# Kernel optimization log

Hardware: AMD Instinct MI355X
Metric: run time of the kernel (lower is better)

## Reference

```python
import jax, jax.numpy as jnp
import numpy as np

DIM_QK = 1024


def setup_inputs() -> dict:
    key = jax.random.key(0)
    ks = jax.random.split(key, 5)
    B, S, D = 4, 2048, 1024
    return {
        "x": jax.random.normal(ks[0], (B, S, D), dtype=jnp.float32),
        "Wq": jax.random.normal(ks[1], (DIM_QK, D), dtype=jnp.float32) * (D ** -0.5),
        "Wk": jax.random.normal(ks[2], (DIM_QK, D), dtype=jnp.float32) * (D ** -0.5),
        "Wv": jax.random.normal(ks[3], (D, D), dtype=jnp.float32) * (D ** -0.5),
        "Wo": jax.random.normal(ks[4], (D, D), dtype=jnp.float32) * (D ** -0.5),
    }


def reference(x, Wq, Wk, Wv, Wo):
    # torch Linear: y = x @ W.T (no bias)
    q = jnp.einsum('bsd,kd->bsk', x, Wq)
    k = jnp.einsum('bsd,kd->bsk', x, Wk)
    v = jnp.einsum('bsd,vd->bsv', x, Wv)
    scale = (DIM_QK // 2) ** (-0.5)
    dist = jnp.einsum('bqk,btk->bqt', q, k) * scale  # [B,S,S]
    weight = jax.lax.stop_gradient(dist)             # pre-softmax scores (detached)
    attn = jax.nn.softmax(dist, axis=-1)
    ctx = jnp.einsum('bqt,btv->bqv', attn, v)
    out = jnp.einsum('bqv,ev->bqe', ctx, Wo)
    return (out, weight)
```

## Files before the change

kernel.cpp:

```cpp
#include <hip/hip_runtime.h>
#include <stdint.h>

typedef __attribute__((ext_vector_type(8))) short bf16x8;
typedef __attribute__((ext_vector_type(4))) float f32x4;

__device__ __forceinline__ unsigned short f32_to_bf16(float f) {
  union { float f; unsigned int u; } v; v.f = f;
  unsigned int u = v.u;
  u += 0x7fffu + ((u >> 16) & 1u);
  return (unsigned short)(u >> 16);
}

__device__ __forceinline__ void gload_lds16(const unsigned short* g, unsigned short* lds_p) {
  __builtin_amdgcn_global_load_lds(
      (const __attribute__((address_space(1))) unsigned int*)g,
      (__attribute__((address_space(3))) unsigned int*)lds_p,
      16, 0, 0);
}

template<int MODE>
__global__ __launch_bounds__(256, 4)
void gemm_bt(const unsigned short* __restrict__ A,
             const unsigned short* __restrict__ Bm,
             void* __restrict__ Cv,
             int M, int N, int K, int lda, int ldb, int ldc,
             long sA_, long sB_, long sC_,
             float scale)
{
  __shared__ unsigned short sA[2 * 128 * 32];
  __shared__ unsigned short sB[2 * 128 * 32];

  const int bz = blockIdx.z;
  const unsigned short* Ab = A + (long)bz * sA_;
  const unsigned short* Bb = Bm + (long)bz * sB_;

  const int nx = gridDim.x;
  const int nwg = nx * gridDim.y;
  const int f = blockIdx.y * nx + blockIdx.x;
  const int cpx = nwg >> 3;
  const int sw = (f & 7) * cpx + (f >> 3);
  const int m0 = (sw % nx) * 128;
  const int n0 = (sw / nx) * 128;

  const int t = threadIdx.x;
  const int lane = t & 63;
  const int w = t >> 6;
  const int wr = (w >> 1) * 64;
  const int wc = (w & 1) * 64;
  const int lrow = lane & 15;
  const int q8s = ((lane >> 4) ^ ((lrow >> 1) & 3)) * 8;

  const int row0 = t >> 2;
  const int kc0 = ((t & 3) ^ ((t >> 3) & 3)) * 8;
  const unsigned short* Ap = Ab + (long)(m0 + row0) * lda + kc0;
  const unsigned short* Bp = Bb + (long)(n0 + row0) * ldb + kc0;
  const long a64 = (long)lda * 64;
  const long b64 = (long)ldb * 64;

  f32x4 acc[4][4];
#pragma unroll
  for (int i = 0; i < 4; ++i)
#pragma unroll
    for (int j = 0; j < 4; ++j)
      acc[i][j] = (f32x4){0.f, 0.f, 0.f, 0.f};

  for (int k0 = 0; k0 < K; k0 += 64) {
    __syncthreads();
#pragma unroll
    for (int s = 0; s < 2; ++s) {
      const int gk = k0 + s * 32;
      gload_lds16(Ap + gk,       &sA[s * 4096 + t * 8]);
      gload_lds16(Ap + a64 + gk, &sA[s * 4096 + t * 8 + 2048]);
      gload_lds16(Bp + gk,       &sB[s * 4096 + t * 8]);
      gload_lds16(Bp + b64 + gk, &sB[s * 4096 + t * 8 + 2048]);
    }
    __syncthreads();

#pragma unroll
    for (int s = 0; s < 2; ++s) {
      bf16x8 af[4], bf[4];
#pragma unroll
      for (int i = 0; i < 4; ++i) {
        af[i] = *(const bf16x8*)&sA[s * 4096 + (wr + i * 16 + lrow) * 32 + q8s];
        bf[i] = *(const bf16x8*)&sB[s * 4096 + (wc + i * 16 + lrow) * 32 + q8s];
      }
#pragma unroll
      for (int mi = 0; mi < 4; ++mi)
#pragma unroll
        for (int ni = 0; ni < 4; ++ni)
          acc[mi][ni] = __builtin_amdgcn_mfma_f32_16x16x32_bf16(af[mi], bf[ni], acc[mi][ni], 0, 0, 0);
    }
  }

  const int cl = lane & 15;
  const int rq = (lane >> 4) * 4;

  if (MODE == 2) {
    float* Cb = (float*)Cv + (long)bz * sC_;
#pragma unroll
    for (int mi = 0; mi < 4; ++mi) {
      const int rowb = m0 + wr + mi * 16 + rq;
#pragma unroll
      for (int ni = 0; ni < 4; ++ni) {
        const int col = n0 + wc + ni * 16 + cl;
#pragma unroll
        for (int r = 0; r < 4; ++r)
          Cb[(long)(rowb + r) * ldc + col] = acc[mi][ni][r] * scale;
      }
    }
  } else {
    unsigned short* Cb = (unsigned short*)Cv + (long)bz * sC_;
#pragma unroll
    for (int mi = 0; mi < 4; ++mi) {
      const int rowb = m0 + wr + mi * 16 + rq;
#pragma unroll
      for (int ni = 0; ni < 4; ++ni) {
        const int col = n0 + wc + ni * 16 + cl;
#pragma unroll
        for (int r = 0; r < 4; ++r)
          Cb[(long)(rowb + r) * ldc + col] = f32_to_bf16(acc[mi][ni][r]);
      }
    }
  }
}

__global__ __launch_bounds__(256)
void softmax_rows(const float* __restrict__ dist, unsigned short* __restrict__ attn) {
  const long row = blockIdx.x;
  const float4* in = (const float4*)(dist + row * 2048);
  const int t = threadIdx.x;
  float4 v0 = in[t];
  float4 v1 = in[t + 256];

  float m = fmaxf(fmaxf(fmaxf(v0.x, v0.y), fmaxf(v0.z, v0.w)),
                  fmaxf(fmaxf(v1.x, v1.y), fmaxf(v1.z, v1.w)));
#pragma unroll
  for (int off = 32; off > 0; off >>= 1)
    m = fmaxf(m, __shfl_xor(m, off, 64));

  __shared__ float redm[4];
  __shared__ float reds[4];
  if ((t & 63) == 0) redm[t >> 6] = m;
  __syncthreads();
  m = fmaxf(fmaxf(redm[0], redm[1]), fmaxf(redm[2], redm[3]));

  float e[8];
  e[0] = __expf(v0.x - m); e[1] = __expf(v0.y - m);
  e[2] = __expf(v0.z - m); e[3] = __expf(v0.w - m);
  e[4] = __expf(v1.x - m); e[5] = __expf(v1.y - m);
  e[6] = __expf(v1.z - m); e[7] = __expf(v1.w - m);

  float s = ((e[0] + e[1]) + (e[2] + e[3])) + ((e[4] + e[5]) + (e[6] + e[7]));
#pragma unroll
  for (int off = 32; off > 0; off >>= 1)
    s += __shfl_xor(s, off, 64);
  if ((t & 63) == 0) reds[t >> 6] = s;
  __syncthreads();
  s = (reds[0] + reds[1]) + (reds[2] + reds[3]);

  const float inv = 1.0f / s;
  ushort4 o0, o1;
  o0.x = f32_to_bf16(e[0] * inv); o0.y = f32_to_bf16(e[1] * inv);
  o0.z = f32_to_bf16(e[2] * inv); o0.w = f32_to_bf16(e[3] * inv);
  o1.x = f32_to_bf16(e[4] * inv); o1.y = f32_to_bf16(e[5] * inv);
  o1.z = f32_to_bf16(e[6] * inv); o1.w = f32_to_bf16(e[7] * inv);
  *(ushort4*)(attn + row * 2048 + t * 4) = o0;
  *(ushort4*)(attn + row * 2048 + 1024 + t * 4) = o1;
}

__global__ __launch_bounds__(256)
void cast_all(const float* __restrict__ Wq, const float* __restrict__ Wk,
              const float* __restrict__ Wv, const float* __restrict__ Wo,
              const float* __restrict__ x, unsigned short* __restrict__ dst) {
  const long i = ((long)blockIdx.x * 256 + threadIdx.x) * 4;
  const float* src;
  long off;
  if (i < 4194304) {
    const int which = (int)(i >> 20);
    src = (which == 0) ? Wq : (which == 1) ? Wk : (which == 2) ? Wv : Wo;
    off = i & 1048575;
  } else {
    src = x;
    off = i - 4194304;
  }
  float4 v = *(const float4*)(src + off);
  ushort4 o;
  o.x = f32_to_bf16(v.x); o.y = f32_to_bf16(v.y);
  o.z = f32_to_bf16(v.z); o.w = f32_to_bf16(v.w);
  *(ushort4*)(dst + i) = o;
}

extern "C" void kernel_launch(void* const* d_in, const int* in_sizes, int n_in,
                              void* d_out, int out_size, void* d_ws, size_t ws_size,
                              hipStream_t stream) {
  const float* x  = (const float*)d_in[0];
  const float* Wq = (const float*)d_in[1];
  const float* Wk = (const float*)d_in[2];
  const float* Wv = (const float*)d_in[3];
  const float* Wo = (const float*)d_in[4];

  const long Bn = 4, S = 2048, D = 1024;
  const long MS = Bn * S;

  float* out_p  = (float*)d_out;
  float* weight = out_p + MS * D;

  unsigned short* Wqb = (unsigned short*)d_ws;
  unsigned short* Wvb = Wqb + 2 * D * D;
  unsigned short* Wob = Wvb + D * D;
  unsigned short* xb  = Wob + D * D;
  unsigned short* qk  = xb + MS * D;
  unsigned short* vtb = qk + MS * 2048;
  unsigned short* attn = qk;
  unsigned short* ctx  = xb;

  cast_all<<<12288, 256, 0, stream>>>(Wq, Wk, Wv, Wo, x, Wqb);

  gemm_bt<0><<<dim3(64, 16, 1), 256, 0, stream>>>(xb, Wqb, qk, 8192, 2048, 1024,
                                                  1024, 1024, 2048, 0, 0, 0, 1.f);
  gemm_bt<0><<<dim3(8, 64, 1), 256, 0, stream>>>(Wvb, xb, vtb, 1024, 8192, 1024,
                                                 1024, 1024, 8192, 0, 0, 0, 1.f);
  gemm_bt<2><<<dim3(16, 16, 4), 256, 0, stream>>>(qk, qk + 1024, weight, 2048, 2048, 1024,
                                                  2048, 2048, 2048,
                                                  S * 2048, S * 2048, S * S,
                                                  0.04419417382415922f);
  softmax_rows<<<(int)(Bn * S), 256, 0, stream>>>(weight, attn);
  gemm_bt<0><<<dim3(16, 8, 4), 256, 0, stream>>>(attn, vtb, ctx, 2048, 1024, 2048,
                                                 2048, 8192, 1024,
                                                 S * S, 2048, S * D, 1.f);
  gemm_bt<2><<<dim3(64, 8, 1), 256, 0, stream>>>(ctx, Wob, out_p, 8192, 1024, 1024,
                                                 1024, 1024, 1024, 0, 0, 0, 1.f);
}
```

Baseline: 333.9 us.

## Stage GEMM epilogue through swizzled LDS for coalesced vector stores

The GEMM epilogue now swaps the MFMA operands so each lane holds four consecutive columns of one row. It stages the tile through a shared 32KB LDS buffer, with two passes for the fp32 mode, and then writes 16-byte coalesced vectors to global memory instead of scattered scalar stores. The XCD-aware block swizzle is removed and launch bounds drop from 4 to 2 waves per EU, presumably to fit the larger LDS footprint and extra registers. The price is extra barriers and LDS traffic in the epilogue, and possibly worse L2 locality across XCDs.

```diff
diff --git a/kernel.cpp b/kernel.cpp
--- a/kernel.cpp
+++ b/kernel.cpp
@@ -19,7 +19,7 @@
 }
 
 template<int MODE>
-__global__ __launch_bounds__(256, 4)
+__global__ __launch_bounds__(256, 2)
 void gemm_bt(const unsigned short* __restrict__ A,
              const unsigned short* __restrict__ Bm,
              void* __restrict__ Cv,
@@ -27,20 +27,16 @@
              long sA_, long sB_, long sC_,
              float scale)
 {
-  __shared__ unsigned short sA[2 * 128 * 32];
-  __shared__ unsigned short sB[2 * 128 * 32];
+  __shared__ unsigned short smem[16384];
+  unsigned short* sA = smem;
+  unsigned short* sB = smem + 8192;
 
   const int bz = blockIdx.z;
   const unsigned short* Ab = A + (long)bz * sA_;
   const unsigned short* Bb = Bm + (long)bz * sB_;
 
-  const int nx = gridDim.x;
-  const int nwg = nx * gridDim.y;
-  const int f = blockIdx.y * nx + blockIdx.x;
-  const int cpx = nwg >> 3;
-  const int sw = (f & 7) * cpx + (f >> 3);
-  const int m0 = (sw % nx) * 128;
-  const int n0 = (sw / nx) * 128;
+  const int m0 = blockIdx.x * 128;
+  const int n0 = blockIdx.y * 128;
 
   const int t = threadIdx.x;
   const int lane = t & 63;
@@ -88,38 +84,74 @@
       for (int mi = 0; mi < 4; ++mi)
 #pragma unroll
         for (int ni = 0; ni < 4; ++ni)
-          acc[mi][ni] = __builtin_amdgcn_mfma_f32_16x16x32_bf16(af[mi], bf[ni], acc[mi][ni], 0, 0, 0);
+          acc[mi][ni] = __builtin_amdgcn_mfma_f32_16x16x32_bf16(bf[ni], af[mi], acc[mi][ni], 0, 0, 0);
     }
   }
 
   const int cl = lane & 15;
   const int rq = (lane >> 4) * 4;
 
+  __syncthreads();
+
   if (MODE == 2) {
+    float* ef = (float*)smem;
     float* Cb = (float*)Cv + (long)bz * sC_;
 #pragma unroll
+    for (int pass = 0; pass < 2; ++pass) {
+      if ((w >> 1) == pass) {
+#pragma unroll
+        for (int mi = 0; mi < 4; ++mi) {
+          const int mr = mi * 16 + cl;
+#pragma unroll
+          for (int ni = 0; ni < 4; ++ni) {
+            const int n16 = (wc + ni * 16 + rq) >> 2;
+            const int ph = n16 ^ (mr & 15);
+            f32x4 v;
+            v[0] = acc[mi][ni][0] * scale; v[1] = acc[mi][ni][1] * scale;
+            v[2] = acc[mi][ni][2] * scale; v[3] = acc[mi][ni][3] * scale;
+            *(f32x4*)&ef[mr * 128 + ph * 4] = v;
+          }
+        }
+      }
+      __syncthreads();
+#pragma unroll
+      for (int i = 0; i < 8; ++i) {
+        const int c = t + i * 256;
+        const int m = c >> 5;
+        const int k16 = c & 31;
+        const int ph = k16 ^ (m & 15);
+        f32x4 v = *(const f32x4*)&ef[m * 128 + ph * 4];
+        *(f32x4*)&Cb[(long)(m0 + pass * 64 + m) * ldc + n0 + k16 * 4] = v;
+      }
+      __syncthreads();
+    }
+  } else {
+    unsigned short* eb = smem;
+    unsigned short* Cb = (unsigned short*)Cv + (long)bz * sC_;
+#pragma unroll
     for (int mi = 0; mi < 4; ++mi) {
-      const int rowb = m0 + wr + mi * 16 + rq;
+      const int mr = wr + mi * 16 + cl;
+      const int sw = (mr & 15) << 1;
 #pragma unroll
       for (int ni = 0; ni < 4; ++ni) {
-        const int col = n0 + wc + ni * 16 + cl;
-#pragma unroll
-        for (int r = 0; r < 4; ++r)
-          Cb[(long)(rowb + r) * ldc + col] = acc[mi][ni][r] * scale;
-      }
-    }
-  } else {
-    unsigned short* Cb = (unsigned short*)Cv + (long)bz * sC_;
-#pragma unroll
-    for (int mi = 0; mi < 4; ++mi) {
-      const int rowb = m0 + wr + mi * 16 + rq;
-#pragma unroll
-      for (int ni = 0; ni < 4; ++ni) {
-        const int col = n0 + wc + ni * 16 + cl;
-#pragma unroll
-        for (int r = 0; r < 4; ++r)
-          Cb[(long)(rowb + r) * ldc + col] = f32_to_bf16(acc[mi][ni][r]);
-      }
+        const int p8 = ((wc + ni * 16 + rq) >> 2) ^ sw;
+        uint2 pk;
+        pk.x = (unsigned)f32_to_bf16(acc[mi][ni][0]) |
+               ((unsigned)f32_to_bf16(acc[mi][ni][1]) << 16);
+        pk.y = (unsigned)f32_to_bf16(acc[mi][ni][2]) |
+               ((unsigned)f32_to_bf16(acc[mi][ni][3]) << 16);
+        *(uint2*)&eb[mr * 128 + p8 * 4] = pk;
+      }
+    }
+    __syncthreads();
+#pragma unroll
+    for (int i = 0; i < 8; ++i) {
+      const int c = t + i * 256;
+      const int m = c >> 4;
+      const int k16 = c & 15;
+      const int ph = k16 ^ (m & 15);
+      bf16x8 v = *(const bf16x8*)&eb[m * 128 + ph * 8];
+      *(bf16x8*)&Cb[(long)(m0 + m) * ldc + n0 + k16 * 8] = v;
     }
   }
 }
```

Result: faster. 315.2 us (-5.6%).
